# Optimization experiments

Measured on AMD Instinct MI355X. Metric: run time of the kernel, lower is better.

The kernel has to match this reference:

```python
import jax, jax.numpy as jnp
import numpy as np

EPS = 1e-5

def conv2d(x, w, b, stride, pad):
    y = jax.lax.conv_general_dilated(x, w, (stride, stride), [(pad, pad), (pad, pad)],
                                     dimension_numbers=('NCHW', 'OIHW', 'NCHW'))
    return y + b[None, :, None, None]

def _sample(xb, py, px):
    # xb: [C,H,W]; py,px: [K,Ho,Wo] fractional sample coords (zero padding outside)
    H, W = xb.shape[1], xb.shape[2]
    y0 = jnp.floor(py); x0 = jnp.floor(px)
    ay = py - y0; ax = px - x0
    y0i = y0.astype(jnp.int32); x0i = x0.astype(jnp.int32)
    out = jnp.zeros((xb.shape[0],) + py.shape, xb.dtype)
    for dy, wy in ((0, 1.0 - ay), (1, ay)):
        for dx, wx in ((0, 1.0 - ax), (1, ax)):
            yi = y0i + dy; xi = x0i + dx
            valid = (yi >= 0) & (yi < H) & (xi >= 0) & (xi < W)
            v = xb[:, jnp.clip(yi, 0, H - 1), jnp.clip(xi, 0, W - 1)]  # [C,K,Ho,Wo]
            out = out + v * (wy * wx * valid)[None]
    return out

def deform_conv2d(x, w, offset, mask, stride, pad):
    # torchvision.ops.deform_conv2d semantics (modulated, 1 offset group)
    B, C, H, W = x.shape
    Co, Ci, kh, kw = w.shape
    K = kh * kw
    Ho = (H + 2 * pad - kh) // stride + 1
    Wo = (W + 2 * pad - kw) // stride + 1
    ky, kx = jnp.meshgrid(jnp.arange(kh), jnp.arange(kw), indexing='ij')
    ky = ky.reshape(K).astype(x.dtype); kx = kx.reshape(K).astype(x.dtype)
    off = offset.reshape(B, K, 2, Ho, Wo)  # channel 2k = dy, 2k+1 = dx
    base_y = (jnp.arange(Ho) * stride - pad).astype(x.dtype)
    base_x = (jnp.arange(Wo) * stride - pad).astype(x.dtype)
    py = base_y[None, None, :, None] + ky[None, :, None, None] + off[:, :, 0]
    px = base_x[None, None, None, :] + kx[None, :, None, None] + off[:, :, 1]
    cols = jax.vmap(_sample)(x, py, px)        # [B,C,K,Ho,Wo]
    cols = cols * mask[:, None]                # modulated
    return jnp.einsum('bckhw,ock->bohw', cols, w.reshape(Co, Ci, K))

def deform_layer(x, off_w, off_b, mod_w, mod_b, w, stride, pad):
    offset = conv2d(x, off_w, off_b, stride, pad)
    mask = 2.0 * jax.nn.sigmoid(conv2d(x, mod_w, mod_b, stride, pad))
    return deform_conv2d(x, w, offset, mask, stride, pad)

def bn(x, g, b, m, v):
    return (x - m[None, :, None, None]) * (g / jnp.sqrt(v + EPS))[None, :, None, None] + b[None, :, None, None]

def prelu(x, alpha):
    return jnp.where(x > 0, x, alpha[None, :, None, None] * x)

def setup_inputs() -> dict:
    key = jax.random.key(0)
    ks = jax.random.split(key, 24)
    B, C, D, H, W, k = 4, 128, 128, 128, 128, 3
    K = k * k
    n = lambda i, shp, s: jax.random.normal(ks[i], shp, dtype=jnp.float32) * s
    inp = {
        'x': n(0, (B, C, H, W), 1.0),
        'bn1_g': 1.0 + n(1, (C,), 0.05), 'bn1_b': n(2, (C,), 0.05),
        'bn1_m': n(3, (C,), 0.1), 'bn1_v': jax.random.uniform(ks[4], (C,), jnp.float32, 0.5, 1.5),
        'off1_w': n(5, (2 * K, C, k, k), 0.01), 'off1_b': n(6, (2 * K,), 0.01),
        'mod1_w': n(7, (K, C, k, k), 0.01), 'mod1_b': n(8, (K,), 0.01),
        'w1': n(9, (D, C, k, k), 1.0 / np.sqrt(C * K)),
        'alpha': jnp.full((D,), 0.25, jnp.float32),
        'off2_w': n(10, (2 * K, D, k, k), 0.01), 'off2_b': n(11, (2 * K,), 0.01),
        'mod2_w': n(12, (K, D, k, k), 0.01), 'mod2_b': n(13, (K,), 0.01),
        'w2': n(14, (D, D, k, k), 1.0 / np.sqrt(D * K)),
        'bn2_g': 1.0 + n(15, (D,), 0.05), 'bn2_b': n(16, (D,), 0.05),
        'bn2_m': n(17, (D,), 0.1), 'bn2_v': jax.random.uniform(ks[18], (D,), jnp.float32, 0.5, 1.5),
    }
    return inp

def reference(x, bn1_g, bn1_b, bn1_m, bn1_v, off1_w, off1_b, mod1_w, mod1_b, w1, alpha,
              off2_w, off2_b, mod2_w, mod2_b, w2, bn2_g, bn2_b, bn2_m, bn2_v):
    # in_channel == depth, stride == 1 -> shortcut is MaxPool2d(1,1) == identity
    shortcut = x
    r = bn(x, bn1_g, bn1_b, bn1_m, bn1_v)
    r = deform_layer(r, off1_w, off1_b, mod1_w, mod1_b, w1, 1, 1)
    r = prelu(r, alpha)
    r = deform_layer(r, off2_w, off2_b, mod2_w, mod2_b, w2, 1, 1)
    r = bn(r, bn2_g, bn2_b, bn2_m, bn2_v)
    return r + shortcut
```

## Files before the change

### kernel.cpp

```cpp
#include <hip/hip_runtime.h>
#include <hip/hip_bf16.h>
#include <hip/hip_fp16.h>
#include <math.h>

#define DEV_INLINE __device__ __forceinline__

typedef __attribute__((ext_vector_type(8))) short short8;
typedef __attribute__((ext_vector_type(8))) unsigned short ushort8v;
typedef __attribute__((ext_vector_type(4))) float f32x4;

constexpr int H = 128, W = 128, C = 128, B = 4;
constexpr int KK = 9;
constexpr int KT2 = 1184;
constexpr int GP = 80;
constexpr int GHALF = 64 * GP;

DEV_INLINE unsigned short f2bf(float f) {
  union { float f; unsigned u; } v; v.f = f;
  unsigned r = v.u + 0x7FFFu + ((v.u >> 16) & 1u);
  return (unsigned short)(r >> 16);
}
DEV_INLINE float ubits(unsigned u) {
  union { unsigned u; float f; } v; v.u = u; return v.f;
}
DEV_INLINE unsigned pack2bf(float a, float b) {
  float2 t; t.x = a; t.y = b;
  __hip_bfloat162 h = __float22bfloat162_rn(t);
  union { __hip_bfloat162 h; unsigned u; } c; c.h = h;
  return c.u;
}
DEV_INLINE unsigned f2h2(float a, float b) {
  __half2 h = __floats2half2_rn(a, b);
  union { __half2 h; unsigned u; } c; c.h = h;
  return c.u;
}
DEV_INLINE float2 h2f2(unsigned u) {
  union { unsigned u; __half2 h; } c; c.u = u;
  return __half22float2(c.h);
}
DEV_INLINE unsigned blend4(unsigned TL, unsigned TR, unsigned BL, unsigned BR,
                           float w00, float w01, float w10, float w11) {
  const float lo = w00 * ubits(TL << 16) + w01 * ubits(TR << 16)
                 + w10 * ubits(BL << 16) + w11 * ubits(BR << 16);
  const float hi = w00 * ubits(TL & 0xFFFF0000u) + w01 * ubits(TR & 0xFFFF0000u)
                 + w10 * ubits(BL & 0xFFFF0000u) + w11 * ubits(BR & 0xFFFF0000u);
  return pack2bf(lo, hi);
}
DEV_INLINE void gload_lds16(const unsigned short* g, unsigned short* l) {
  __builtin_amdgcn_global_load_lds(
      (const __attribute__((address_space(1))) unsigned*)g,
      (__attribute__((address_space(3))) unsigned*)l, 16, 0, 0);
}

template<int LAYER>
__global__ __launch_bounds__(256, 4)
void fusedL(const unsigned short* __restrict__ src,
            const unsigned short* __restrict__ wOM,
            const unsigned short* __restrict__ wS,
            const float* __restrict__ bias,
            const float* __restrict__ pA, const float* __restrict__ pB,
            const float* __restrict__ pM, const float* __restrict__ pV,
            const float* __restrict__ resid,
            unsigned short* __restrict__ outh,
            float* __restrict__ outf)
{
  constexpr bool BN   = (LAYER == 1);
  constexpr int  NCH3 = BN ? 37 : 36;
  __shared__ __attribute__((aligned(16))) char smem[33536];
  float* sOff = (float*)smem;
  unsigned short* aBuf0 = (unsigned short*)smem;
  unsigned short* aBuf1 = (unsigned short*)(smem + 8192);
  char* gBuf = smem + 16384;
  unsigned* sTabU = (unsigned*)(smem + 26624);

  const int tid  = threadIdx.x;
  const int lane = tid & 63;
  const int m16  = lane & 15;
  const int q    = lane >> 4;
  const int wv   = tid >> 6;

  const int raw  = blockIdx.x;
  const int xcd  = raw & 7;
  const int slot = raw >> 3;
  const int b    = xcd >> 1;
  const int hy   = ((xcd & 1) << 6) | (slot >> 1);
  const int hx0  = (slot & 1) << 6;
  const unsigned short* __restrict__ srcB = src + ((size_t)b << 14) * C;

  const int pos  = (wv << 4) + m16;
  const int ppos = tid >> 2;
  const int ps   = tid & 3;

  f32x4 acc2[2];
  acc2[0] = (f32x4){0.f, 0.f, 0.f, 0.f};
  acc2[1] = (f32x4){0.f, 0.f, 0.f, 0.f};

  {
    const int iy = hy - 1, ix = hx0 + ppos - 1;
    uint4 v; v.x = 0; v.y = 0; v.z = 0; v.w = 0;
    if (((unsigned)iy < (unsigned)H) && ((unsigned)ix < (unsigned)W))
      v = *(const uint4*)(srcB + (size_t)(iy * W + ix) * C + (ps << 3));
    *(uint4*)(gBuf + ppos * GP + (ps << 4)) = v;
  }
  short8 pa0 = *(const short8*)(wOM + (size_t)lane * 8);
  short8 pa1 = *(const short8*)(wOM + (size_t)lane * 8 + 512);
  __syncthreads();

  #pragma unroll 1
  for (int ch = 0; ch < 36; ++ch) {
    const short8 a0 = pa0, a1 = pa1;
    if (ch + 1 < 36) {
      const unsigned short* ap = wOM + ((size_t)((ch + 1) * 128 + lane)) * 8;
      pa0 = *(const short8*)(ap);
      pa1 = *(const short8*)(ap + 512);
    }
    uint4 nv; nv.x = 0; nv.y = 0; nv.z = 0; nv.w = 0;
    if (ch + 1 < 36) {
      const int tapn = (ch + 1) >> 2, cgn = (ch + 1) & 3;
      const int ky = tapn / 3, kx = tapn - 3 * (tapn / 3);
      const int iy = hy + ky - 1;
      const int ix = hx0 + ppos + kx - 1;
      if (((unsigned)iy < (unsigned)H) && ((unsigned)ix < (unsigned)W))
        nv = *(const uint4*)(srcB + (size_t)(iy * W + ix) * C + (cgn << 5) + (ps << 3));
    }
    const short8 bfrg = *(const short8*)(gBuf + (ch & 1) * GHALF + pos * GP + (q << 4));
    acc2[0] = __builtin_amdgcn_mfma_f32_16x16x32_bf16(a0, bfrg, acc2[0], 0, 0, 0);
    acc2[1] = __builtin_amdgcn_mfma_f32_16x16x32_bf16(a1, bfrg, acc2[1], 0, 0, 0);
    if (ch + 1 < 36) {
      *(uint4*)(gBuf + ((ch + 1) & 1) * GHALF + ppos * GP + (ps << 4)) = nv;
      __syncthreads();
    }
  }
  if constexpr (BN) {
    union { unsigned u[4]; short8 s; } bfr;
    float sv[8];
    #pragma unroll
    for (int j = 0; j < 8; ++j) {
      const int kj = (q << 3) + j;
      float s = 0.f;
      if (kj < KK) {
        const int ky = kj / 3, kx = kj - 3 * (kj / 3);
        const int iy = hy + ky - 1, ix = hx0 + pos + kx - 1;
        s = (((unsigned)iy < (unsigned)H) && ((unsigned)ix < (unsigned)W)) ? 1.f : 0.f;
      }
      sv[j] = s;
    }
    #pragma unroll
    for (int t = 0; t < 4; ++t) bfr.u[t] = pack2bf(sv[2 * t], sv[2 * t + 1]);
    const unsigned short* ap = wOM + ((size_t)36 * 128 + lane) * 8;
    acc2[0] = __builtin_amdgcn_mfma_f32_16x16x32_bf16(*(const short8*)(ap), bfr.s, acc2[0], 0, 0, 0);
    acc2[1] = __builtin_amdgcn_mfma_f32_16x16x32_bf16(*(const short8*)(ap + 512), bfr.s, acc2[1], 0, 0, 0);
  }
  __syncthreads();
  #pragma unroll
  for (int ot = 0; ot < 2; ++ot) {
    #pragma unroll
    for (int rg = 0; rg < 4; ++rg) {
      const int o = ot * 16 + (q << 2) + rg;
      if (o < 27) {
        float v = acc2[ot][rg] + bias[o];
        if (o >= 18) v = 2.f / (1.f + expf(-v));
        sOff[pos * 29 + o] = v;
      }
    }
  }
  __syncthreads();

  {
    const float* myOff = sOff + pos * 29;
    #pragma unroll
    for (int tap = 0; tap < 9; ++tap) {
      const int ky = tap / 3, kx = tap - 3 * (tap / 3);
      const float oy = myOff[2 * tap];
      const float ox = myOff[2 * tap + 1];
      const float mv = myOff[18 + tap];
      const float py = (float)(hy - 1 + ky) + oy;
      const float px = (float)(hx0 + pos - 1 + kx) + ox;
      const float fy = floorf(py), fx = floorf(px);
      const float ay = py - fy, ax = px - fx;
      const int y0 = (int)fy, x0 = (int)fx;
      const int y1 = y0 + 1, x1 = x0 + 1;
      const float wyt = (1.f - ay) * (((unsigned)y0 < (unsigned)H) ? 1.f : 0.f);
      const float wyb = ay * (((unsigned)y1 < (unsigned)H) ? 1.f : 0.f);
      const int y0c = min(max(y0, 0), H - 1), y1c = min(max(y1, 0), H - 1);
      const int bx  = min(max(x0, 0), W - 2);
      float wA = 0.f, wB = 0.f;
      if (x0 == bx)          { wA = 1.f - ax; wB = ax; }
      else if (x1 == bx)     { wA = ax; }
      else if (x0 == bx + 1) { wB = 1.f - ax; }
      if (q == 0) {
        const int tb = (tap * 64 + pos) * 3;
        sTabU[tb + 0] = (unsigned)(y0c * W + bx) | ((unsigned)(y1c * W + bx) << 16);
        sTabU[tb + 1] = f2h2(mv * wyt * wA, mv * wyt * wB);
        sTabU[tb + 2] = f2h2(mv * wyb * wA, mv * wyb * wB);
      }
    }
  }
  __syncthreads();

  f32x4 acc[2][4];
  #pragma unroll
  for (int i = 0; i < 2; ++i)
    #pragma unroll
    for (int j = 0; j < 4; ++j) acc[i][j] = (f32x4){0.f, 0.f, 0.f, 0.f};

  {
    unsigned short* dst0 = aBuf0 + (wv << 9);
    gload_lds16(wS + (size_t)tid * 8, dst0);
    gload_lds16(wS + (size_t)(256 + tid) * 8, dst0 + 2048);
  }
  unsigned pid, pw0, pw1;
  {
    const int tb = ppos * 3;
    pid = sTabU[tb]; pw0 = sTabU[tb + 1]; pw1 = sTabU[tb + 2];
    const unsigned short* pT  = srcB + (size_t)(pid & 0xFFFFu) * C + (ps << 3);
    const unsigned short* pBm = srcB + (size_t)(pid >> 16) * C + (ps << 3);
    const uint4 TL = *(const uint4*)(pT),  TR = *(const uint4*)(pT + C);
    const uint4 BL = *(const uint4*)(pBm), BR = *(const uint4*)(pBm + C);
    const float2 wa = h2f2(pw0), wb = h2f2(pw1);
    uint4 o;
    o.x = blend4(TL.x, TR.x, BL.x, BR.x, wa.x, wa.y, wb.x, wb.y);
    o.y = blend4(TL.y, TR.y, BL.y, BR.y, wa.x, wa.y, wb.x, wb.y);
    o.z = blend4(TL.z, TR.z, BL.z, BR.z, wa.x, wa.y, wb.x, wb.y);
    o.w = blend4(TL.w, TR.w, BL.w, BR.w, wa.x, wa.y, wb.x, wb.y);
    *(uint4*)(gBuf + ppos * GP + (ps << 4)) = o;
  }
  __syncthreads();

  #pragma unroll 1
  for (int ch = 0; ch < 36; ++ch) {
    const int p = ch & 1;
    const bool morew = (ch + 1 < NCH3);
    const bool morep = (ch + 1 < 36);
    if (morew) {
      unsigned short* wd = ((ch + 1) & 1) ? aBuf1 : aBuf0;
      unsigned short* dst = wd + (wv << 9);
      const size_t gb = (size_t)(ch + 1) * 4096;
      gload_lds16(wS + gb + (size_t)tid * 8, dst);
      gload_lds16(wS + gb + (size_t)(256 + tid) * 8, dst + 2048);
    }
    if (morep && (((ch + 1) & 3) == 0)) {
      const int tb = (((ch + 1) >> 2) * 64 + ppos) * 3;
      pid = sTabU[tb]; pw0 = sTabU[tb + 1]; pw1 = sTabU[tb + 2];
    }
    uint4 TL, TR, BL, BR;
    if (morep) {
      const int cbn = (((ch + 1) & 3) << 5) + (ps << 3);
      const unsigned short* pT  = srcB + (size_t)(pid & 0xFFFFu) * C + cbn;
      const unsigned short* pBm = srcB + (size_t)(pid >> 16) * C + cbn;
      TL = *(const uint4*)(pT);  TR = *(const uint4*)(pT + C);
      BL = *(const uint4*)(pBm); BR = *(const uint4*)(pBm + C);
    }
    const unsigned short* rbuf = p ? aBuf1 : aBuf0;
    const short8 af0 = *(const short8*)(rbuf + ((size_t)((2 * wv) * 64 + lane)) * 8);
    const short8 af1 = *(const short8*)(rbuf + ((size_t)((2 * wv + 1) * 64 + lane)) * 8);
    const char* gb = gBuf + p * GHALF;
    short8 bf[4];
    #pragma unroll
    for (int pg = 0; pg < 4; ++pg)
      bf[pg] = *(const short8*)(gb + (pg * 16 + m16) * GP + (q << 4));
    #pragma unroll
    for (int pg = 0; pg < 4; ++pg) {
      acc[0][pg] = __builtin_amdgcn_mfma_f32_16x16x32_bf16(af0, bf[pg], acc[0][pg], 0, 0, 0);
      acc[1][pg] = __builtin_amdgcn_mfma_f32_16x16x32_bf16(af1, bf[pg], acc[1][pg], 0, 0, 0);
    }
    if (morep) {
      const float2 wa = h2f2(pw0), wb = h2f2(pw1);
      uint4 o;
      o.x = blend4(TL.x, TR.x, BL.x, BR.x, wa.x, wa.y, wb.x, wb.y);
      o.y = blend4(TL.y, TR.y, BL.y, BR.y, wa.x, wa.y, wb.x, wb.y);
      o.z = blend4(TL.z, TR.z, BL.z, BR.z, wa.x, wa.y, wb.x, wb.y);
      o.w = blend4(TL.w, TR.w, BL.w, BR.w, wa.x, wa.y, wb.x, wb.y);
      *(uint4*)(gBuf + (p ^ 1) * GHALF + ppos * GP + (ps << 4)) = o;
    }
    if (morew) __syncthreads();
  }

  if constexpr (BN) {
    const short8 af0 = *(const short8*)(aBuf0 + ((size_t)((2 * wv) * 64 + lane)) * 8);
    const short8 af1 = *(const short8*)(aBuf0 + ((size_t)((2 * wv + 1) * 64 + lane)) * 8);
    #pragma unroll
    for (int pg = 0; pg < 4; ++pg) {
      float sv[8];
      #pragma unroll
      for (int j = 0; j < 8; ++j) {
        const int k = (q << 3) + j;
        float s = 0.f;
        if (k < KK) {
          const int tb = (k * 64 + pg * 16 + m16) * 3;
          const float2 a = h2f2(sTabU[tb + 1]);
          const float2 c = h2f2(sTabU[tb + 2]);
          s = a.x + a.y + c.x + c.y;
        }
        sv[j] = s;
      }
      union { unsigned u[4]; short8 s; } bfr;
      #pragma unroll
      for (int t = 0; t < 4; ++t) bfr.u[t] = pack2bf(sv[2 * t], sv[2 * t + 1]);
      acc[0][pg] = __builtin_amdgcn_mfma_f32_16x16x32_bf16(af0, bfr.s, acc[0][pg], 0, 0, 0);
      acc[1][pg] = __builtin_amdgcn_mfma_f32_16x16x32_bf16(af1, bfr.s, acc[1][pg], 0, 0, 0);
    }
  }

  #pragma unroll
  for (int oi = 0; oi < 2; ++oi) {
    const int ot = wv * 2 + oi;
    if constexpr (LAYER == 1) {
      const float a0 = pA[ot * 16 + (q << 2) + 0];
      const float a1 = pA[ot * 16 + (q << 2) + 1];
      const float a2 = pA[ot * 16 + (q << 2) + 2];
      const float a3 = pA[ot * 16 + (q << 2) + 3];
      #pragma unroll
      for (int pg = 0; pg < 4; ++pg) {
        const float v0 = acc[oi][pg][0], v1 = acc[oi][pg][1];
        const float v2 = acc[oi][pg][2], v3 = acc[oi][pg][3];
        uint2 st;
        st.x = pack2bf(v0 > 0.f ? v0 : a0 * v0, v1 > 0.f ? v1 : a1 * v1);
        st.y = pack2bf(v2 > 0.f ? v2 : a2 * v2, v3 > 0.f ? v3 : a3 * v3);
        const int n = (b << 14) + hy * W + hx0 + pg * 16 + m16;
        *(uint2*)(outh + (size_t)n * C + ot * 16 + (q << 2)) = st;
      }
    } else {
      #pragma unroll
      for (int rg = 0; rg < 4; ++rg) {
        const int o = ot * 16 + (q << 2) + rg;
        const float s  = pA[o] * rsqrtf(pV[o] + 1e-5f);
        const float sh = pB[o] - pM[o] * s;
        #pragma unroll
        for (int pg = 0; pg < 4; ++pg) {
          const size_t oi2 = (((size_t)(b * C + o)) << 14) + hy * W + hx0 + pg * 16 + m16;
          outf[oi2] = acc[oi][pg][rg] * s + sh + resid[oi2];
        }
      }
    }
  }
}

__global__ __launch_bounds__(256, 4)
void xcvt3(const float* __restrict__ x, unsigned short* __restrict__ xb)
{
  __shared__ unsigned tile[64 * 69];
  const int b   = blockIdx.y;
  const int p0  = blockIdx.x * 64;
  const int tid = threadIdx.x;
  const int pl  = tid & 63;
  const int cg  = tid >> 6;
  const float* __restrict__ xp = x + (((size_t)(b * C) + cg * 32) << 14) + p0 + pl;
  #pragma unroll
  for (int j = 0; j < 16; ++j) {
    const float a = xp[(size_t)(2 * j) << 14];
    const float c = xp[(size_t)(2 * j + 1) << 14];
    tile[pl * 69 + cg * 16 + j] = pack2bf(a, c);
  }
  __syncthreads();
  const int pl2 = tid >> 2;
  const int cq  = tid & 3;
  unsigned* dst = (unsigned*)(xb + (((size_t)(b << 14)) + p0 + pl2) * C + cq * 32);
  #pragma unroll
  for (int k = 0; k < 16; k += 4) {
    uint4 v;
    v.x = tile[pl2 * 69 + cq * 16 + k];
    v.y = tile[pl2 * 69 + cq * 16 + k + 1];
    v.z = tile[pl2 * 69 + cq * 16 + k + 2];
    v.w = tile[pl2 * 69 + cq * 16 + k + 3];
    *(uint4*)(dst + k) = v;
  }
}

__global__ void prep5(const float* __restrict__ w1, const float* __restrict__ w2,
                      const float* __restrict__ ow1, const float* __restrict__ mw1,
                      const float* __restrict__ ob1, const float* __restrict__ mb1,
                      const float* __restrict__ ow2, const float* __restrict__ mw2,
                      const float* __restrict__ ob2, const float* __restrict__ mb2,
                      const float* __restrict__ g, const float* __restrict__ bb,
                      const float* __restrict__ m, const float* __restrict__ v,
                      unsigned short* __restrict__ wb1, unsigned short* __restrict__ wb2,
                      unsigned short* __restrict__ wom1, unsigned short* __restrict__ wom2,
                      float* __restrict__ bias1, float* __restrict__ bias2)
{
  const int i = blockIdx.x * 256 + threadIdx.x;
  if (i < 128 * KT2) {
    const int j = i & 7, lane = (i >> 3) & 63, ot = (i >> 9) & 7, ch = i >> 12;
    const int o = ot * 16 + (lane & 15);
    const int qj = ((lane >> 4) << 3) + j;
    unsigned short v1 = 0, v2 = 0;
    if (ch < 36) {
      const int tap = ch >> 2;
      const int c   = ((ch & 3) << 5) + qj;
      const float s = g[c] * rsqrtf(v[c] + 1e-5f);
      v1 = f2bf(w1[(size_t)(o * 128 + c) * 9 + tap] * s);
      v2 = f2bf(w2[(size_t)(o * 128 + c) * 9 + tap]);
    } else if (qj < KK) {
      float acc = 0.f;
      for (int c = 0; c < 128; ++c) {
        const float s  = g[c] * rsqrtf(v[c] + 1e-5f);
        const float sh = bb[c] - m[c] * s;
        acc += w1[(size_t)(o * 128 + c) * 9 + qj] * sh;
      }
      v1 = f2bf(acc);
    }
    wb1[i] = v1; wb2[i] = v2;
  }
  if (i < 32 * KT2) {
    const int j = i & 7, lane = (i >> 3) & 63, ot = (i >> 9) & 1, ch = i >> 10;
    const int o = ot * 16 + (lane & 15);
    const int qj = ((lane >> 4) << 3) + j;
    unsigned short v1 = 0, v2 = 0;
    if (ch < 36) {
      const int tap = ch >> 2;
      const int c   = ((ch & 3) << 5) + qj;
      const float s = g[c] * rsqrtf(v[c] + 1e-5f);
      if (o < 18) {
        v1 = f2bf(ow1[(size_t)(o * 128 + c) * 9 + tap] * s);
        v2 = f2bf(ow2[(size_t)(o * 128 + c) * 9 + tap]);
      } else if (o < 27) {
        v1 = f2bf(mw1[(size_t)((o - 18) * 128 + c) * 9 + tap] * s);
        v2 = f2bf(mw2[(size_t)((o - 18) * 128 + c) * 9 + tap]);
      }
    } else if (qj < KK && o < 27) {
      const float* wsrc = (o < 18) ? ow1 + (size_t)o * 1152
                                   : mw1 + (size_t)(o - 18) * 1152;
      float acc = 0.f;
      for (int c = 0; c < 128; ++c) {
        const float s  = g[c] * rsqrtf(v[c] + 1e-5f);
        const float sh = bb[c] - m[c] * s;
        acc += wsrc[(size_t)c * 9 + qj] * sh;
      }
      v1 = f2bf(acc);
    }
    wom1[i] = v1; wom2[i] = v2;
  }
  if (i < 32) {
    float b1 = 0.f, b2 = 0.f;
    if (i < 18)      { b1 = ob1[i];      b2 = ob2[i]; }
    else if (i < 27) { b1 = mb1[i - 18]; b2 = mb2[i - 18]; }
    bias1[i] = b1; bias2[i] = b2;
  }
}

extern "C" void kernel_launch(void* const* d_in, const int* in_sizes, int n_in,
                              void* d_out, int out_size, void* d_ws, size_t ws_size,
                              hipStream_t stream)
{
  const float* x     = (const float*)d_in[0];
  const float* bn1g  = (const float*)d_in[1];
  const float* bn1b  = (const float*)d_in[2];
  const float* bn1m  = (const float*)d_in[3];
  const float* bn1v  = (const float*)d_in[4];
  const float* ow1   = (const float*)d_in[5];
  const float* ob1   = (const float*)d_in[6];
  const float* mw1   = (const float*)d_in[7];
  const float* mb1   = (const float*)d_in[8];
  const float* w1    = (const float*)d_in[9];
  const float* alpha = (const float*)d_in[10];
  const float* ow2   = (const float*)d_in[11];
  const float* ob2   = (const float*)d_in[12];
  const float* mw2   = (const float*)d_in[13];
  const float* mb2   = (const float*)d_in[14];
  const float* w2    = (const float*)d_in[15];
  const float* bn2g  = (const float*)d_in[16];
  const float* bn2b  = (const float*)d_in[17];
  const float* bn2m  = (const float*)d_in[18];
  const float* bn2v  = (const float*)d_in[19];
  float* out = (float*)d_out;

  char* wsp = (char*)d_ws;
  unsigned short* xbf  = (unsigned short*)(wsp);
  unsigned short* r2bf = (unsigned short*)(wsp + 16777216);
  unsigned short* wb1  = (unsigned short*)(wsp + 40632320);
  unsigned short* wb2  = (unsigned short*)(wsp + 40935424);
  unsigned short* wom1 = (unsigned short*)(wsp + 41238528);
  unsigned short* wom2 = (unsigned short*)(wsp + 41314304);
  float* bias1 = (float*)(wsp + 41390080);
  float* bias2 = (float*)(wsp + 41390208);

  xcvt3<<<dim3(256, 4), 256, 0, stream>>>(x, xbf);
  prep5<<<(128 * KT2 + 255) / 256, 256, 0, stream>>>(
      w1, w2, ow1, mw1, ob1, mb1, ow2, mw2, ob2, mb2,
      bn1g, bn1b, bn1m, bn1v, wb1, wb2, wom1, wom2, bias1, bias2);

  fusedL<1><<<1024, 256, 0, stream>>>(xbf, wom1, wb1, bias1, alpha,
      nullptr, nullptr, nullptr, nullptr, r2bf, nullptr);
  fusedL<2><<<1024, 256, 0, stream>>>(r2bf, wom2, wb2, bias2, bn2g,
      bn2b, bn2m, bn2v, x, nullptr, out);
}
```

Baseline: 274.1 us.

## Deepen software pipeline and load main-conv weights directly into registers

Both fused conv loops now prefetch their global inputs two chunks ahead and hold them in registers, so each load has a full iteration to land before it is blended or stored to LDS. The main deformable conv no longer stages weight tiles into LDS with global_load_lds; each wave reads its own A fragments straight from global into registers. That frees roughly half the shared memory and lets the barrier wait only on LDS counters (lgkmcnt) rather than on all outstanding memory ops. The cost is higher register pressure, which could hurt occupancy at 4 blocks per CU, and more redundant global weight traffic served by cache.

```diff
diff --git a/kernel.cpp b/kernel.cpp
--- a/kernel.cpp
+++ b/kernel.cpp
@@ -46,10 +46,10 @@
                  + w10 * ubits(BL & 0xFFFF0000u) + w11 * ubits(BR & 0xFFFF0000u);
   return pack2bf(lo, hi);
 }
-DEV_INLINE void gload_lds16(const unsigned short* g, unsigned short* l) {
-  __builtin_amdgcn_global_load_lds(
-      (const __attribute__((address_space(1))) unsigned*)g,
-      (__attribute__((address_space(3))) unsigned*)l, 16, 0, 0);
+DEV_INLINE void lgkm_barrier() {
+  asm volatile("s_waitcnt lgkmcnt(0)" ::: "memory");
+  __builtin_amdgcn_s_barrier();
+  __builtin_amdgcn_sched_barrier(0);
 }
 
 template<int LAYER>
@@ -66,12 +66,10 @@
 {
   constexpr bool BN   = (LAYER == 1);
   constexpr int  NCH3 = BN ? 37 : 36;
-  __shared__ __attribute__((aligned(16))) char smem[33536];
+  __shared__ __attribute__((aligned(16))) char smem[17152];
+  char* gBuf = smem;
   float* sOff = (float*)smem;
-  unsigned short* aBuf0 = (unsigned short*)smem;
-  unsigned short* aBuf1 = (unsigned short*)(smem + 8192);
-  char* gBuf = smem + 16384;
-  unsigned* sTabU = (unsigned*)(smem + 26624);
+  unsigned* sTabU = (unsigned*)(smem + 10240);
 
   const int tid  = threadIdx.x;
   const int lane = tid & 63;
@@ -102,34 +100,41 @@
       v = *(const uint4*)(srcB + (size_t)(iy * W + ix) * C + (ps << 3));
     *(uint4*)(gBuf + ppos * GP + (ps << 4)) = v;
   }
+  uint4 pendV; pendV.x = 0; pendV.y = 0; pendV.z = 0; pendV.w = 0;
+  {
+    const int iy = hy - 1, ix = hx0 + ppos - 1;
+    if (((unsigned)iy < (unsigned)H) && ((unsigned)ix < (unsigned)W))
+      pendV = *(const uint4*)(srcB + (size_t)(iy * W + ix) * C + 32 + (ps << 3));
+  }
   short8 pa0 = *(const short8*)(wOM + (size_t)lane * 8);
   short8 pa1 = *(const short8*)(wOM + (size_t)lane * 8 + 512);
-  __syncthreads();
-
-  #pragma unroll 1
+  lgkm_barrier();
+
+  #pragma unroll 2
   for (int ch = 0; ch < 36; ++ch) {
+    const int p = ch & 1;
     const short8 a0 = pa0, a1 = pa1;
     if (ch + 1 < 36) {
       const unsigned short* ap = wOM + ((size_t)((ch + 1) * 128 + lane)) * 8;
       pa0 = *(const short8*)(ap);
       pa1 = *(const short8*)(ap + 512);
     }
-    uint4 nv; nv.x = 0; nv.y = 0; nv.z = 0; nv.w = 0;
-    if (ch + 1 < 36) {
-      const int tapn = (ch + 1) >> 2, cgn = (ch + 1) & 3;
-      const int ky = tapn / 3, kx = tapn - 3 * (tapn / 3);
+    uint4 newV; newV.x = 0; newV.y = 0; newV.z = 0; newV.w = 0;
+    if (ch + 2 < 36) {
+      const int t2 = (ch + 2) >> 2, c2 = (ch + 2) & 3;
+      const int ky = t2 / 3, kx = t2 - 3 * (t2 / 3);
       const int iy = hy + ky - 1;
       const int ix = hx0 + ppos + kx - 1;
       if (((unsigned)iy < (unsigned)H) && ((unsigned)ix < (unsigned)W))
-        nv = *(const uint4*)(srcB + (size_t)(iy * W + ix) * C + (cgn << 5) + (ps << 3));
-    }
-    const short8 bfrg = *(const short8*)(gBuf + (ch & 1) * GHALF + pos * GP + (q << 4));
+        newV = *(const uint4*)(srcB + (size_t)(iy * W + ix) * C + (c2 << 5) + (ps << 3));
+    }
+    if (ch + 1 < 36)
+      *(uint4*)(gBuf + (p ^ 1) * GHALF + ppos * GP + (ps << 4)) = pendV;
+    const short8 bfrg = *(const short8*)(gBuf + p * GHALF + pos * GP + (q << 4));
     acc2[0] = __builtin_amdgcn_mfma_f32_16x16x32_bf16(a0, bfrg, acc2[0], 0, 0, 0);
     acc2[1] = __builtin_amdgcn_mfma_f32_16x16x32_bf16(a1, bfrg, acc2[1], 0, 0, 0);
-    if (ch + 1 < 36) {
-      *(uint4*)(gBuf + ((ch + 1) & 1) * GHALF + ppos * GP + (ps << 4)) = nv;
-      __syncthreads();
-    }
+    pendV = newV;
+    if (ch + 1 < 36) lgkm_barrier();
   }
   if constexpr (BN) {
     union { unsigned u[4]; short8 s; } bfr;
@@ -204,20 +209,17 @@
     #pragma unroll
     for (int j = 0; j < 4; ++j) acc[i][j] = (f32x4){0.f, 0.f, 0.f, 0.f};
 
-  {
-    unsigned short* dst0 = aBuf0 + (wv << 9);
-    gload_lds16(wS + (size_t)tid * 8, dst0);
-    gload_lds16(wS + (size_t)(256 + tid) * 8, dst0 + 2048);
-  }
-  unsigned pid, pw0, pw1;
+  unsigned tabId, tabW0, tabW1;
   {
     const int tb = ppos * 3;
-    pid = sTabU[tb]; pw0 = sTabU[tb + 1]; pw1 = sTabU[tb + 2];
-    const unsigned short* pT  = srcB + (size_t)(pid & 0xFFFFu) * C + (ps << 3);
-    const unsigned short* pBm = srcB + (size_t)(pid >> 16) * C + (ps << 3);
+    tabId = sTabU[tb]; tabW0 = sTabU[tb + 1]; tabW1 = sTabU[tb + 2];
+  }
+  {
+    const unsigned short* pT  = srcB + (size_t)(tabId & 0xFFFFu) * C + (ps << 3);
+    const unsigned short* pBm = srcB + (size_t)(tabId >> 16) * C + (ps << 3);
     const uint4 TL = *(const uint4*)(pT),  TR = *(const uint4*)(pT + C);
     const uint4 BL = *(const uint4*)(pBm), BR = *(const uint4*)(pBm + C);
-    const float2 wa = h2f2(pw0), wb = h2f2(pw1);
+    const float2 wa = h2f2(tabW0), wb = h2f2(tabW1);
     uint4 o;
     o.x = blend4(TL.x, TR.x, BL.x, BR.x, wa.x, wa.y, wb.x, wb.y);
     o.y = blend4(TL.y, TR.y, BL.y, BR.y, wa.x, wa.y, wb.x, wb.y);
@@ -225,35 +227,54 @@
     o.w = blend4(TL.w, TR.w, BL.w, BR.w, wa.x, wa.y, wb.x, wb.y);
     *(uint4*)(gBuf + ppos * GP + (ps << 4)) = o;
   }
-  __syncthreads();
-
-  #pragma unroll 1
+  uint4 pTL, pTR, pBL, pBR;
+  {
+    const int cbn = 32 + (ps << 3);
+    const unsigned short* pT  = srcB + (size_t)(tabId & 0xFFFFu) * C + cbn;
+    const unsigned short* pBm = srcB + (size_t)(tabId >> 16) * C + cbn;
+    pTL = *(const uint4*)(pT);  pTR = *(const uint4*)(pT + C);
+    pBL = *(const uint4*)(pBm); pBR = *(const uint4*)(pBm + C);
+  }
+  short8 pa0_, pa1_;
+  {
+    const unsigned short* ap = wS + ((size_t)((2 * wv) * 64 + lane)) * 8;
+    pa0_ = *(const short8*)(ap);
+    pa1_ = *(const short8*)(ap + 512);
+  }
+  lgkm_barrier();
+
+  #pragma unroll 2
   for (int ch = 0; ch < 36; ++ch) {
     const int p = ch & 1;
-    const bool morew = (ch + 1 < NCH3);
-    const bool morep = (ch + 1 < 36);
-    if (morew) {
-      unsigned short* wd = ((ch + 1) & 1) ? aBuf1 : aBuf0;
-      unsigned short* dst = wd + (wv << 9);
-      const size_t gb = (size_t)(ch + 1) * 4096;
-      gload_lds16(wS + gb + (size_t)tid * 8, dst);
-      gload_lds16(wS + gb + (size_t)(256 + tid) * 8, dst + 2048);
-    }
-    if (morep && (((ch + 1) & 3) == 0)) {
-      const int tb = (((ch + 1) >> 2) * 64 + ppos) * 3;
-      pid = sTabU[tb]; pw0 = sTabU[tb + 1]; pw1 = sTabU[tb + 2];
-    }
-    uint4 TL, TR, BL, BR;
-    if (morep) {
-      const int cbn = (((ch + 1) & 3) << 5) + (ps << 3);
-      const unsigned short* pT  = srcB + (size_t)(pid & 0xFFFFu) * C + cbn;
-      const unsigned short* pBm = srcB + (size_t)(pid >> 16) * C + cbn;
-      TL = *(const uint4*)(pT);  TR = *(const uint4*)(pT + C);
-      BL = *(const uint4*)(pBm); BR = *(const uint4*)(pBm + C);
-    }
-    const unsigned short* rbuf = p ? aBuf1 : aBuf0;
-    const short8 af0 = *(const short8*)(rbuf + ((size_t)((2 * wv) * 64 + lane)) * 8);
-    const short8 af1 = *(const short8*)(rbuf + ((size_t)((2 * wv + 1) * 64 + lane)) * 8);
+    const short8 af0 = pa0_, af1 = pa1_;
+    if (ch + 1 < NCH3) {
+      const unsigned short* ap = wS + ((size_t)((ch + 1) * 4096)) +
+                                 ((size_t)((2 * wv) * 64 + lane)) * 8;
+      pa0_ = *(const short8*)(ap);
+      pa1_ = *(const short8*)(ap + 512);
+    }
+    unsigned ntId = tabId, ntW0 = tabW0, ntW1 = tabW1;
+    if ((((ch + 2) & 3) == 0) && (ch + 2 < 36)) {
+      const int tb = (((ch + 2) >> 2) * 64 + ppos) * 3;
+      ntId = sTabU[tb]; ntW0 = sTabU[tb + 1]; ntW1 = sTabU[tb + 2];
+    }
+    uint4 nTL = pTL, nTR = pTR, nBL = pBL, nBR = pBR;
+    if (ch + 2 < 36) {
+      const int cbn = (((ch + 2) & 3) << 5) + (ps << 3);
+      const unsigned short* pT  = srcB + (size_t)(ntId & 0xFFFFu) * C + cbn;
+      const unsigned short* pBm = srcB + (size_t)(ntId >> 16) * C + cbn;
+      nTL = *(const uint4*)(pT);  nTR = *(const uint4*)(pT + C);
+      nBL = *(const uint4*)(pBm); nBR = *(const uint4*)(pBm + C);
+    }
+    if (ch + 1 < 36) {
+      const float2 wa = h2f2(tabW0), wb = h2f2(tabW1);
+      uint4 o;
+      o.x = blend4(pTL.x, pTR.x, pBL.x, pBR.x, wa.x, wa.y, wb.x, wb.y);
+      o.y = blend4(pTL.y, pTR.y, pBL.y, pBR.y, wa.x, wa.y, wb.x, wb.y);
+      o.z = blend4(pTL.z, pTR.z, pBL.z, pBR.z, wa.x, wa.y, wb.x, wb.y);
+      o.w = blend4(pTL.w, pTR.w, pBL.w, pBR.w, wa.x, wa.y, wb.x, wb.y);
+      *(uint4*)(gBuf + (p ^ 1) * GHALF + ppos * GP + (ps << 4)) = o;
+    }
     const char* gb = gBuf + p * GHALF;
     short8 bf[4];
     #pragma unroll
@@ -264,21 +285,13 @@
       acc[0][pg] = __builtin_amdgcn_mfma_f32_16x16x32_bf16(af0, bf[pg], acc[0][pg], 0, 0, 0);
       acc[1][pg] = __builtin_amdgcn_mfma_f32_16x16x32_bf16(af1, bf[pg], acc[1][pg], 0, 0, 0);
     }
-    if (morep) {
-      const float2 wa = h2f2(pw0), wb = h2f2(pw1);
-      uint4 o;
-      o.x = blend4(TL.x, TR.x, BL.x, BR.x, wa.x, wa.y, wb.x, wb.y);
-      o.y = blend4(TL.y, TR.y, BL.y, BR.y, wa.x, wa.y, wb.x, wb.y);
-      o.z = blend4(TL.z, TR.z, BL.z, BR.z, wa.x, wa.y, wb.x, wb.y);
-      o.w = blend4(TL.w, TR.w, BL.w, BR.w, wa.x, wa.y, wb.x, wb.y);
-      *(uint4*)(gBuf + (p ^ 1) * GHALF + ppos * GP + (ps << 4)) = o;
-    }
-    if (morew) __syncthreads();
+    pTL = nTL; pTR = nTR; pBL = nBL; pBR = nBR;
+    tabId = ntId; tabW0 = ntW0; tabW1 = ntW1;
+    if (ch + 1 < 36) lgkm_barrier();
   }
 
   if constexpr (BN) {
-    const short8 af0 = *(const short8*)(aBuf0 + ((size_t)((2 * wv) * 64 + lane)) * 8);
-    const short8 af1 = *(const short8*)(aBuf0 + ((size_t)((2 * wv + 1) * 64 + lane)) * 8);
+    const short8 af0 = pa0_, af1 = pa1_;
     #pragma unroll
     for (int pg = 0; pg < 4; ++pg) {
       float sv[8];
```

After: 257.7 us. 6.0% less time.
